# Performance work log

Hardware: AMD Instinct MI355X
Metric: run time of the kernel (lower is better)

Reference implementation:

```python
import jax, jax.numpy as jnp
import numpy as np

N = 100000   # nodes per node type
E = 1000000  # edges per edge type
C = 128      # channels
H = 4        # num_heads
D = C // H   # head_dim


def setup_inputs() -> dict:
    key = jax.random.key(0)
    ks = jax.random.split(key, 16)
    return {
        "x_A": jax.random.normal(ks[0], (N, C), jnp.float32),
        "x_B": jax.random.normal(ks[1], (N, C), jnp.float32),
        "Wq": jax.random.normal(ks[2], (C, C), jnp.float32) * 0.05,
        "bq": jax.random.normal(ks[3], (C,), jnp.float32) * 0.05,
        "Wk": jax.random.normal(ks[4], (C, C), jnp.float32) * 0.05,
        "bk": jax.random.normal(ks[5], (C,), jnp.float32) * 0.05,
        "Wv": jax.random.normal(ks[6], (C, C), jnp.float32) * 0.05,
        "bv": jax.random.normal(ks[7], (C,), jnp.float32) * 0.05,
        "gamma": jnp.ones((C,), jnp.float32),
        "beta": jnp.zeros((C,), jnp.float32),
        "bias_AB": jax.random.normal(ks[8], (1,), jnp.float32),
        "bias_BA": jax.random.normal(ks[9], (1,), jnp.float32),
        "sb_AB": jax.random.normal(ks[10], (E,), jnp.float32),
        "sb_BA": jax.random.normal(ks[11], (E,), jnp.float32),
        "edge_index_AB": jax.random.randint(ks[12], (2, E), 0, N, jnp.int32),
        "edge_index_BA": jax.random.randint(ks[13], (2, E), 0, N, jnp.int32),
    }


def _edge_attention(x_src, x_dst, src, dst, sb, etype_bias, Wq, bq, Wk, bk, Wv, bv):
    """Per-edge-type attention: gather -> score -> dst-segment softmax -> scatter-add."""
    n_dst = x_dst.shape[0]
    Q = (x_dst @ Wq.T + bq).reshape(n_dst, H, D)
    K = (x_src @ Wk.T + bk).reshape(-1, H, D)
    V = (x_src @ Wv.T + bv).reshape(-1, H, D)
    # [E, H] per-edge scores
    scores = jnp.einsum('ehd,ehd->eh', Q[dst], K[src]) / np.float32(np.sqrt(D))
    scores = scores + sb[:, None] + etype_bias  # spatial bias + edge-type bias
    # segment softmax over edges grouped by dst node (numerically stable)
    m = jax.ops.segment_max(scores, dst, num_segments=n_dst)
    ex = jnp.exp(scores - m[dst])
    denom = jax.ops.segment_sum(ex, dst, num_segments=n_dst)
    w = ex / denom[dst]  # [E, H]
    msg = (V[src] * w[:, :, None]).reshape(-1, C)  # [E, C]
    return jax.ops.segment_sum(msg, dst, num_segments=n_dst)  # index_add_


def _layernorm(x, gamma, beta, eps=1e-5):
    mu = x.mean(-1, keepdims=True)
    var = ((x - mu) ** 2).mean(-1, keepdims=True)
    return (x - mu) / jnp.sqrt(var + eps) * gamma + beta


def _forward(x_A, x_B, Wq, bq, Wk, bk, Wv, bv, gamma, beta,
             bias_AB, bias_BA, sb_AB, sb_BA, edge_index_AB, edge_index_BA):
    src_ab, dst_ab = edge_index_AB[0], edge_index_AB[1]  # A -> B
    src_ba, dst_ba = edge_index_BA[0], edge_index_BA[1]  # B -> A
    lin = (Wq, bq, Wk, bk, Wv, bv)
    out_B = _edge_attention(x_A, x_B, src_ab, dst_ab, sb_AB, bias_AB, *lin)
    out_A = _edge_attention(x_B, x_A, src_ba, dst_ba, sb_BA, bias_BA, *lin)
    # total degree = in_deg + out_deg per node type
    ones_e = jnp.ones((E,), jnp.float32)
    deg_A = (jax.ops.segment_sum(ones_e, src_ab, num_segments=N)
             + jax.ops.segment_sum(ones_e, dst_ba, num_segments=N))
    deg_B = (jax.ops.segment_sum(ones_e, dst_ab, num_segments=N)
             + jax.ops.segment_sum(ones_e, src_ba, num_segments=N))
    out_A = out_A + deg_A[:, None]
    out_B = out_B + deg_B[:, None]
    out_A = _layernorm(out_A + x_A, gamma, beta)
    out_B = _layernorm(out_B + x_B, gamma, beta)
    return out_A, out_B


def reference(x_A, x_B, Wq, bq, Wk, bk, Wv, bv, gamma, beta,
              bias_AB, bias_BA, sb_AB, sb_BA, edge_index_AB, edge_index_BA):
    return _forward(x_A, x_B, Wq, bq, Wk, bk, Wv, bv, gamma, beta,
                    bias_AB, bias_BA, sb_AB, sb_BA, edge_index_AB, edge_index_BA)
```

## Files before the change

### kernel.cpp

```cpp
#include <hip/hip_runtime.h>

#define CH 128
#define QSCALE (0.17677669529663687f * 1.4426950408889634f)
#define LOG2E 1.4426950408889634f
#define SCAN_BLK 1024
#define KVSTRIDE 384
#define QROWS 32

typedef _Float16 f16;
typedef _Float16 f16x2 __attribute__((ext_vector_type(2)));
typedef _Float16 f16x8 __attribute__((ext_vector_type(8)));
typedef __attribute__((ext_vector_type(4))) float f32x4;

__device__ __forceinline__ unsigned pk2(float a, float b) {
    auto h = __builtin_amdgcn_cvt_pkrtz(a, b);
    return __builtin_bit_cast(unsigned, h);
}
__device__ __forceinline__ f16x2 u2h(unsigned u) { return __builtin_bit_cast(f16x2, u); }

template <int CTRL>
__device__ __forceinline__ float dpp_add(float x) {
    const int t = __builtin_amdgcn_update_dpp(0, __builtin_bit_cast(int, x), CTRL, 0xF, 0xF, false);
    return x + __builtin_bit_cast(float, t);
}
__device__ __forceinline__ float head_sum(float x) {
    x = dpp_add<0xB1>(x);
    x = dpp_add<0x4E>(x);
    x = dpp_add<0x124>(x);
    x = dpp_add<0x128>(x);
    return x;
}

__global__ __launch_bounds__(256) void wcvt(const float* __restrict__ Wq, const float* __restrict__ Wk,
                                            const float* __restrict__ Wv, unsigned short* __restrict__ out)
{
    const int i = blockIdx.x * 256 + threadIdx.x;
    if (i >= 3 * CH * CH) return;
    const float* W = (i < CH * CH) ? Wq : (i < 2 * CH * CH) ? Wk : Wv;
    const float s = (i < CH * CH) ? QSCALE : 1.f;
    f16 h = (f16)(W[i & (CH * CH - 1)] * s);
    out[i] = __builtin_bit_cast(unsigned short, h);
}

__global__ __launch_bounds__(256) void qkv_mfma(
    const float* __restrict__ xA, const float* __restrict__ xB,
    const unsigned short* __restrict__ Wb,
    const float* __restrict__ bq, const float* __restrict__ bk, const float* __restrict__ bv,
    unsigned short* __restrict__ Qb,
    unsigned char* __restrict__ KVb,
    int n)
{
    __shared__ __align__(16) char lds[8192];
    const int type = blockIdx.y;
    const float* x = type ? xB : xA;
    const int bRow = blockIdx.x * QROWS;
    const int tid = threadIdx.x;

    #pragma unroll
    for (int j = 0; j < 4; ++j) {
        const int flat16 = j * 256 + tid;
        const int row = flat16 >> 5;
        const int c16 = flat16 & 31;
        float4 v = make_float4(0.f, 0.f, 0.f, 0.f);
        if (bRow + row < n) v = *(const float4*)(x + (size_t)(bRow + row) * CH + c16 * 4);
        const int off = (row * 256 + c16 * 8) ^ ((row & 7) << 4);
        *(uint2*)(lds + off) = make_uint2(pk2(v.x, v.y), pk2(v.z, v.w));
    }
    __syncthreads();

    const int w = tid >> 6, l = tid & 63, lr = l & 15, lg = l >> 4;
    const int colbase = w * 32;

    f32x4 acc[3][2][2];
    #pragma unroll
    for (int p = 0; p < 3; ++p)
        #pragma unroll
        for (int ct = 0; ct < 2; ++ct)
            #pragma unroll
            for (int rt = 0; rt < 2; ++rt)
                acc[p][ct][rt] = (f32x4){0.f, 0.f, 0.f, 0.f};

    #pragma unroll
    for (int kt = 0; kt < 4; ++kt) {
        f16x8 bx[2];
        #pragma unroll
        for (int rt = 0; rt < 2; ++rt) {
            const int row = rt * 16 + lr;
            const int off = (row * 256 + kt * 64 + lg * 16) ^ ((row & 7) << 4);
            bx[rt] = *(const f16x8*)(lds + off);
        }
        #pragma unroll
        for (int p = 0; p < 3; ++p) {
            #pragma unroll
            for (int ct = 0; ct < 2; ++ct) {
                const int ocol = colbase + ct * 16 + lr;
                const f16x8 a = *(const f16x8*)(Wb + ((size_t)p << 14) + (size_t)ocol * CH + kt * 32 + lg * 8);
                #pragma unroll
                for (int rt = 0; rt < 2; ++rt)
                    acc[p][ct][rt] = __builtin_amdgcn_mfma_f32_16x16x32_f16(a, bx[rt], acc[p][ct][rt], 0, 0, 0);
            }
        }
    }

    unsigned short* Qo = Qb + (size_t)type * n * CH;
    unsigned char* KVo = KVb + (size_t)type * n * KVSTRIDE;

    #pragma unroll
    for (int p = 0; p < 3; ++p) {
        __syncthreads();
        const float* bias = (p == 0) ? bq : (p == 1) ? bk : bv;
        #pragma unroll
        for (int ct = 0; ct < 2; ++ct) {
            const int c0 = colbase + ct * 16 + lg * 4;
            float4 bb = *(const float4*)(bias + c0);
            if (p == 0) { bb.x *= QSCALE; bb.y *= QSCALE; bb.z *= QSCALE; bb.w *= QSCALE; }
            #pragma unroll
            for (int rt = 0; rt < 2; ++rt) {
                const int nl = rt * 16 + lr;
                const int swz = (nl & 7) << 4;
                const f32x4 a4 = acc[p][ct][rt];
                if (p == 1) {
                    const int cbk = w * 32 + ct * 16 + lg * 4;
                    int kw = __builtin_amdgcn_cvt_pk_fp8_f32(a4[0] + bb.x, a4[1] + bb.y, 0, false);
                    kw     = __builtin_amdgcn_cvt_pk_fp8_f32(a4[2] + bb.z, a4[3] + bb.w, kw, true);
                    *(unsigned*)(lds + nl * 128 + (cbk ^ swz)) = (unsigned)kw;
                } else {
                    const int cbq = w * 64 + ct * 32 + lg * 8;
                    *(uint2*)(lds + nl * 256 + (cbq ^ swz)) =
                        make_uint2(pk2(a4[0] + bb.x, a4[1] + bb.y), pk2(a4[2] + bb.z, a4[3] + bb.w));
                }
            }
        }
        __syncthreads();
        if (p == 1) {
            const int row = tid >> 3, c = tid & 7;
            const uint4 val = *(const uint4*)(lds + row * 128 + ((c ^ (row & 7)) << 4));
            const int node = bRow + row;
            if (node < n) *(uint4*)(KVo + (size_t)node * KVSTRIDE + c * 16) = val;
        } else {
            #pragma unroll
            for (int j = 0; j < 2; ++j) {
                const int flat = j * 256 + tid;
                const int row = flat >> 4, c16 = flat & 15;
                const uint4 val = *(const uint4*)(lds + row * 256 + ((c16 ^ (row & 7)) << 4));
                const int node = bRow + row;
                if (node < n) {
                    if (p == 0) *(uint4*)(Qo + (size_t)node * CH + c16 * 8) = val;
                    else        *(uint4*)(KVo + (size_t)node * KVSTRIDE + 128 + c16 * 16) = val;
                }
            }
        }
    }
}

__global__ __launch_bounds__(256) void deg_hist(const int* __restrict__ eiAB, const int* __restrict__ eiBA,
                                                int* __restrict__ degAB, int* __restrict__ degBA,
                                                int nE, int ebl)
{
    const int dir = blockIdx.x >= ebl;
    const int e = ((blockIdx.x - dir * ebl) * 256 + threadIdx.x) * 4;
    if (e >= nE) return;
    const int* ei = dir ? eiBA : eiAB;
    int* deg = dir ? degBA : degAB;
    if (e + 3 < nE) {
        const int4 d4 = *(const int4*)(ei + nE + e);
        atomicAdd(&deg[d4.x], 1); atomicAdd(&deg[d4.y], 1);
        atomicAdd(&deg[d4.z], 1); atomicAdd(&deg[d4.w], 1);
    } else {
        for (int j = e; j < nE; ++j) atomicAdd(&deg[ei[nE + j]], 1);
    }
}

__global__ __launch_bounds__(256) void scan_local(const int* __restrict__ degAB, const int* __restrict__ degBA,
                                                  int* __restrict__ offsAB, int* __restrict__ offsBA,
                                                  int* __restrict__ bsums, int n, int nb)
{
    __shared__ int s[256];
    const int dir = blockIdx.x >= nb;
    const int blk = blockIdx.x - dir * nb;
    const int* deg = dir ? degBA : degAB;
    int* offs = dir ? offsBA : offsAB;
    int* bs = bsums + dir * 256;

    const int t = threadIdx.x;
    const int base = blk * SCAN_BLK + t * 4;
    int v0 = 0, v1 = 0, v2 = 0, v3 = 0;
    if (base + 3 < n) {
        int4 q = *(const int4*)(deg + base);
        v0 = q.x; v1 = q.y; v2 = q.z; v3 = q.w;
    } else {
        if (base + 0 < n) v0 = deg[base + 0];
        if (base + 1 < n) v1 = deg[base + 1];
        if (base + 2 < n) v2 = deg[base + 2];
    }
    const int tsum = v0 + v1 + v2 + v3;
    s[t] = tsum;
    __syncthreads();
    for (int off = 1; off < 256; off <<= 1) {
        int add = (t >= off) ? s[t - off] : 0;
        __syncthreads();
        s[t] += add;
        __syncthreads();
    }
    const int excl = s[t] - tsum;
    if (base + 0 < n) offs[base + 0] = excl;
    if (base + 1 < n) offs[base + 1] = excl + v0;
    if (base + 2 < n) offs[base + 2] = excl + v0 + v1;
    if (base + 3 < n) offs[base + 3] = excl + v0 + v1 + v2;
    if (t == 255) bs[blk] = s[255];
}

__global__ __launch_bounds__(256) void add_bsums(int* __restrict__ offsAB, int* __restrict__ offsBA,
                                                 int* __restrict__ curAB, int* __restrict__ curBA,
                                                 const int* __restrict__ bsums, int n, int nbl, int nb)
{
    __shared__ int s[256];
    const int dir = blockIdx.x >= nbl;
    const int blk = blockIdx.x - dir * nbl;
    const int t = threadIdx.x;
    int v = (t < nb) ? bsums[dir * 256 + t] : 0;
    s[t] = v;
    __syncthreads();
    for (int off = 1; off < 256; off <<= 1) {
        int add = (t >= off) ? s[t - off] : 0;
        __syncthreads();
        s[t] += add;
        __syncthreads();
    }
    const int i = blk * 256 + t;
    if (i >= n) return;
    const int bi = i >> 10;
    const int excl = (bi == 0) ? 0 : s[bi - 1];
    int* offs = dir ? offsBA : offsAB;
    int* cur  = dir ? curBA  : curAB;
    const int vv = offs[i] + excl;
    offs[i] = vv;
    cur[i] = vv;
}

__global__ __launch_bounds__(256) void csr_fill(const int* __restrict__ eiAB, const int* __restrict__ eiBA,
                                                const float* __restrict__ sbAB, const float* __restrict__ sbBA,
                                                const float* __restrict__ biasAB, const float* __restrict__ biasBA,
                                                int* __restrict__ curAB, int* __restrict__ curBA,
                                                int2* __restrict__ edAB, int2* __restrict__ edBA,
                                                int nE, int ebl)
{
    const int dir = blockIdx.x >= ebl;
    const int e = ((blockIdx.x - dir * ebl) * 256 + threadIdx.x) * 4;
    if (e >= nE) return;
    const int* ei = dir ? eiBA : eiAB;
    const float* sb = dir ? sbBA : sbAB;
    const float bia = dir ? biasBA[0] : biasAB[0];
    int* cur = dir ? curBA : curAB;
    int2* ed = dir ? edBA : edAB;
    if (e + 3 < nE) {
        const int4 s4 = *(const int4*)(ei + e);
        const int4 d4 = *(const int4*)(ei + nE + e);
        const float4 b4 = *(const float4*)(sb + e);
        int p0 = atomicAdd(&cur[d4.x], 1); ed[p0] = make_int2(s4.x * KVSTRIDE, __float_as_int((b4.x + bia) * LOG2E));
        int p1 = atomicAdd(&cur[d4.y], 1); ed[p1] = make_int2(s4.y * KVSTRIDE, __float_as_int((b4.y + bia) * LOG2E));
        int p2 = atomicAdd(&cur[d4.z], 1); ed[p2] = make_int2(s4.z * KVSTRIDE, __float_as_int((b4.z + bia) * LOG2E));
        int p3 = atomicAdd(&cur[d4.w], 1); ed[p3] = make_int2(s4.w * KVSTRIDE, __float_as_int((b4.w + bia) * LOG2E));
    } else {
        for (int j = e; j < nE; ++j) {
            const int pos = atomicAdd(&cur[ei[nE + j]], 1);
            ed[pos] = make_int2(ei[j] * KVSTRIDE, __float_as_int((sb[j] + bia) * LOG2E));
        }
    }
}

__global__ __launch_bounds__(256) void attn_node(
    const unsigned short* __restrict__ Qb,
    const unsigned char* __restrict__ KVb,
    const float* __restrict__ xA, const float* __restrict__ xB,
    const int* __restrict__ offsAB, const int* __restrict__ offsBA,
    const int* __restrict__ degAB, const int* __restrict__ degBA,
    const int2* __restrict__ edAB, const int2* __restrict__ edBA,
    const float* __restrict__ gamma, const float* __restrict__ beta,
    float* __restrict__ out, int n, int abl)
{
    const int dir = blockIdx.x >= abl;
    const int node = (blockIdx.x - dir * abl) * 4 + (threadIdx.x >> 6);
    if (node >= n) return;
    const int l = threadIdx.x & 63;
    const int l2 = l * 2;

    const unsigned short* Q = Qb + (size_t)dir * n * CH;
    const unsigned char* KV = KVb + (size_t)(1 - dir) * n * KVSTRIDE;
    const float* x = dir ? xB : xA;
    const int* offs = dir ? offsAB : offsBA;
    const int* deg  = dir ? degAB  : degBA;
    const int2* ed  = dir ? edAB   : edBA;
    float* o = out + (size_t)dir * n * CH;

    const f16x2 qp = u2h(*(const unsigned*)(Q + (size_t)node * CH + l2));
    const float qf0 = (float)qp[0], qf1 = (float)qp[1];

    const int beg = __builtin_amdgcn_readfirstlane(offs[node]);
    const int d   = __builtin_amdgcn_readfirstlane(deg[node]);

    float m = -3.0e38f, den = 0.f;
    f16x2 a01 = (f16x2){(f16)0.f, (f16)0.f};

    auto loadE = [&](int i, float& sbf, unsigned& kc, unsigned& vc) {
        if (i < d) {
            const int2 e = ed[beg + i];
            sbf = __int_as_float(e.y);
            const unsigned b = (unsigned)e.x;
            kc = *(const unsigned short*)(KV + b + l2);
            vc = *(const unsigned*)(KV + b + 128 + l2 * 2);
        } else {
            sbf = __int_as_float((int)0xFF800000u);
            kc = 0; vc = 0;
        }
    };

    auto procPair = [&](float sf0, unsigned k0, unsigned v0,
                        float sf1, unsigned k1, unsigned v1) {
        const auto kf0 = __builtin_amdgcn_cvt_pk_f32_fp8((int)k0, false);
        const auto kf1 = __builtin_amdgcn_cvt_pk_f32_fp8((int)k1, false);
        float sa = head_sum(fmaf(qf0, kf0[0], qf1 * kf0[1])) + sf0;
        float sb = head_sum(fmaf(qf0, kf1[0], qf1 * kf1[1])) + sf1;
        const float pm = fmaxf(sa, sb);
        if (!__all(pm <= m + 8.f)) {
            const float mn = fmaxf(m, pm);
            const float sc = exp2f(m - mn);
            den *= sc;
            a01 *= u2h(pk2(sc, sc));
            m = mn;
        }
        const float ea = exp2f(sa - m);
        const float eb = exp2f(sb - m);
        den += ea + eb;
        a01 += u2h(pk2(ea, ea)) * u2h(v0);
        a01 += u2h(pk2(eb, eb)) * u2h(v1);
    };

    float sA0, sA1, sA2, sA3, sB0, sB1, sB2, sB3;
    unsigned kA0, kA1, kA2, kA3, kB0, kB1, kB2, kB3;
    unsigned vA0, vA1, vA2, vA3, vB0, vB1, vB2, vB3;
    loadE(0, sA0, kA0, vA0); loadE(1, sA1, kA1, vA1);
    loadE(2, sA2, kA2, vA2); loadE(3, sA3, kA3, vA3);
    loadE(4, sB0, kB0, vB0); loadE(5, sB1, kB1, vB1);
    loadE(6, sB2, kB2, vB2); loadE(7, sB3, kB3, vB3);

    for (int i = 0; i < d; i += 8) {
        procPair(sA0, kA0, vA0, sA1, kA1, vA1);
        procPair(sA2, kA2, vA2, sA3, kA3, vA3);
        loadE(i + 8,  sA0, kA0, vA0); loadE(i + 9,  sA1, kA1, vA1);
        loadE(i + 10, sA2, kA2, vA2); loadE(i + 11, sA3, kA3, vA3);
        if (i + 4 >= d) break;
        procPair(sB0, kB0, vB0, sB1, kB1, vB1);
        procPair(sB2, kB2, vB2, sB3, kB3, vB3);
        loadE(i + 12, sB0, kB0, vB0); loadE(i + 13, sB1, kB1, vB1);
        loadE(i + 14, sB2, kB2, vB2); loadE(i + 15, sB3, kB3, vB3);
    }

    const float inv = (den > 0.f) ? 1.f / den : 0.f;
    const float2 xv = *(const float2*)(x + (size_t)node * CH + l2);
    const float w0 = (float)a01[0] * inv + xv.x;
    const float w1 = (float)a01[1] * inv + xv.y;

    float sum = w0 + w1;
    #pragma unroll
    for (int off = 32; off; off >>= 1) sum += __shfl_xor(sum, off);
    const float mean = sum * (1.f / 128.f);
    const float c0 = w0 - mean, c1 = w1 - mean;
    float vs = c0 * c0 + c1 * c1;
    #pragma unroll
    for (int off = 32; off; off >>= 1) vs += __shfl_xor(vs, off);
    const float rstd = rsqrtf(vs * (1.f / 128.f) + 1e-5f);

    const float2 g = *(const float2*)(gamma + l2);
    const float2 bt = *(const float2*)(beta + l2);
    float2 ov;
    ov.x = c0 * rstd * g.x + bt.x;
    ov.y = c1 * rstd * g.y + bt.y;
    *(float2*)(o + (size_t)node * CH + l2) = ov;
}

extern "C" void kernel_launch(void* const* d_in, const int* in_sizes, int n_in,
                              void* d_out, int out_size, void* d_ws, size_t ws_size,
                              hipStream_t stream)
{
    const float* xA     = (const float*)d_in[0];
    const float* xB     = (const float*)d_in[1];
    const float* Wq     = (const float*)d_in[2];
    const float* bq     = (const float*)d_in[3];
    const float* Wk     = (const float*)d_in[4];
    const float* bk     = (const float*)d_in[5];
    const float* Wv     = (const float*)d_in[6];
    const float* bv     = (const float*)d_in[7];
    const float* gamma  = (const float*)d_in[8];
    const float* beta   = (const float*)d_in[9];
    const float* biasAB = (const float*)d_in[10];
    const float* biasBA = (const float*)d_in[11];
    const float* sbAB   = (const float*)d_in[12];
    const float* sbBA   = (const float*)d_in[13];
    const int*   eiAB   = (const int*)d_in[14];
    const int*   eiBA   = (const int*)d_in[15];

    const int n  = in_sizes[0] / CH;
    const int nE = in_sizes[12];
    const size_t NC = (size_t)n * CH;

    char* p = (char*)d_ws;
    auto carve = [&](size_t bytes) { char* r = p; p += (bytes + 15) & ~(size_t)15; return r; };
    unsigned short* Qb = (unsigned short*)carve(2 * NC * 2);
    unsigned char*  KVb = (unsigned char*)carve((size_t)2 * n * KVSTRIDE);
    unsigned short* Wb  = (unsigned short*)carve(3 * CH * CH * 2);
    int2* edAB  = (int2*)carve((size_t)nE * 8);
    int2* edBA  = (int2*)carve((size_t)nE * 8);
    int* offsAB = (int*)carve((size_t)n * 4);
    int* offsBA = (int*)carve((size_t)n * 4);
    int* degAB  = (int*)carve((size_t)2 * n * 4);
    int* degBA  = degAB + n;
    int* curAB  = (int*)carve((size_t)n * 4);
    int* curBA  = (int*)carve((size_t)n * 4);
    int* bsums  = (int*)carve(2 * 256 * 4);

    float* out = (float*)d_out;

    (void)hipMemsetAsync(degAB, 0, (size_t)2 * n * sizeof(int), stream);

    wcvt<<<(3 * CH * CH + 255) / 256, 256, 0, stream>>>(Wq, Wk, Wv, Wb);

    const int ebl4 = (nE + 1023) / 1024;
    deg_hist<<<2 * ebl4, 256, 0, stream>>>(eiAB, eiBA, degAB, degBA, nE, ebl4);

    dim3 qkv_grid((n + QROWS - 1) / QROWS, 2);
    qkv_mfma<<<qkv_grid, 256, 0, stream>>>(xA, xB, Wb, bq, bk, bv, Qb, KVb, n);

    const int nb = (n + SCAN_BLK - 1) / SCAN_BLK;
    scan_local<<<2 * nb, 256, 0, stream>>>(degAB, degBA, offsAB, offsBA, bsums, n, nb);
    const int nbl = (n + 255) / 256;
    add_bsums<<<2 * nbl, 256, 0, stream>>>(offsAB, offsBA, curAB, curBA, bsums, n, nbl, nb);

    csr_fill<<<2 * ebl4, 256, 0, stream>>>(eiAB, eiBA, sbAB, sbBA, biasAB, biasBA,
                                           curAB, curBA, edAB, edBA, nE, ebl4);

    const int abl = (n + 3) / 4;
    attn_node<<<2 * abl, 256, 0, stream>>>(Qb, KVb, xA, xB, offsAB, offsBA, degAB, degBA,
                                           edAB, edBA, gamma, beta, out, n, abl);
}
```

Measured before the change: 508.3 us.

## Merge weight conversion with degree histogram and QKV GEMM with CSR fill

Folds the weight-conversion kernel into the degree-histogram launch, and runs the QKV MFMA projection and the CSR fill as disjoint block ranges of one launch. The goal is fewer kernel launches and letting the compute-bound GEMM overlap the atomic-bound scatter, which previously ran serially. The QKV grid is flattened, with the node type taken from the low bit of blockIdx. In exchange, the fused kernels carry the GEMM's shared-memory footprint on the scatter blocks, and blocks with different resource use now compete for the same CUs.

```diff
diff --git a/kernel.cpp b/kernel.cpp
--- a/kernel.cpp
+++ b/kernel.cpp
@@ -6,6 +6,7 @@
 #define SCAN_BLK 1024
 #define KVSTRIDE 384
 #define QROWS 32
+#define WCVT_BLOCKS 192
 
 typedef _Float16 f16;
 typedef _Float16 f16x2 __attribute__((ext_vector_type(2)));
@@ -31,29 +32,148 @@
     return x;
 }
 
-__global__ __launch_bounds__(256) void wcvt(const float* __restrict__ Wq, const float* __restrict__ Wk,
-                                            const float* __restrict__ Wv, unsigned short* __restrict__ out)
-{
-    const int i = blockIdx.x * 256 + threadIdx.x;
-    if (i >= 3 * CH * CH) return;
-    const float* W = (i < CH * CH) ? Wq : (i < 2 * CH * CH) ? Wk : Wv;
-    const float s = (i < CH * CH) ? QSCALE : 1.f;
-    f16 h = (f16)(W[i & (CH * CH - 1)] * s);
-    out[i] = __builtin_bit_cast(unsigned short, h);
-}
-
-__global__ __launch_bounds__(256) void qkv_mfma(
+__global__ __launch_bounds__(256) void wcvt_hist(
+    const float* __restrict__ Wq, const float* __restrict__ Wk, const float* __restrict__ Wv,
+    unsigned short* __restrict__ Wb,
+    const int* __restrict__ eiAB, const int* __restrict__ eiBA,
+    int* __restrict__ degAB, int* __restrict__ degBA,
+    int nE, int ebl)
+{
+    if ((int)blockIdx.x < WCVT_BLOCKS) {
+        const int i = blockIdx.x * 256 + threadIdx.x;
+        const float* W = (i < CH * CH) ? Wq : (i < 2 * CH * CH) ? Wk : Wv;
+        const float s = (i < CH * CH) ? QSCALE : 1.f;
+        f16 h = (f16)(W[i & (CH * CH - 1)] * s);
+        Wb[i] = __builtin_bit_cast(unsigned short, h);
+        return;
+    }
+    const int b = blockIdx.x - WCVT_BLOCKS;
+    const int dir = b >= ebl;
+    const int e = ((b - dir * ebl) * 256 + threadIdx.x) * 4;
+    if (e >= nE) return;
+    const int* ei = dir ? eiBA : eiAB;
+    int* deg = dir ? degBA : degAB;
+    if (e + 3 < nE) {
+        const int4 d4 = *(const int4*)(ei + nE + e);
+        atomicAdd(&deg[d4.x], 1); atomicAdd(&deg[d4.y], 1);
+        atomicAdd(&deg[d4.z], 1); atomicAdd(&deg[d4.w], 1);
+    } else {
+        for (int j = e; j < nE; ++j) atomicAdd(&deg[ei[nE + j]], 1);
+    }
+}
+
+__global__ __launch_bounds__(256) void scan_local(const int* __restrict__ degAB, const int* __restrict__ degBA,
+                                                  int* __restrict__ offsAB, int* __restrict__ offsBA,
+                                                  int* __restrict__ bsums, int n, int nb)
+{
+    __shared__ int s[256];
+    const int dir = blockIdx.x >= nb;
+    const int blk = blockIdx.x - dir * nb;
+    const int* deg = dir ? degBA : degAB;
+    int* offs = dir ? offsBA : offsAB;
+    int* bs = bsums + dir * 256;
+
+    const int t = threadIdx.x;
+    const int base = blk * SCAN_BLK + t * 4;
+    int v0 = 0, v1 = 0, v2 = 0, v3 = 0;
+    if (base + 3 < n) {
+        int4 q = *(const int4*)(deg + base);
+        v0 = q.x; v1 = q.y; v2 = q.z; v3 = q.w;
+    } else {
+        if (base + 0 < n) v0 = deg[base + 0];
+        if (base + 1 < n) v1 = deg[base + 1];
+        if (base + 2 < n) v2 = deg[base + 2];
+    }
+    const int tsum = v0 + v1 + v2 + v3;
+    s[t] = tsum;
+    __syncthreads();
+    for (int off = 1; off < 256; off <<= 1) {
+        int add = (t >= off) ? s[t - off] : 0;
+        __syncthreads();
+        s[t] += add;
+        __syncthreads();
+    }
+    const int excl = s[t] - tsum;
+    if (base + 0 < n) offs[base + 0] = excl;
+    if (base + 1 < n) offs[base + 1] = excl + v0;
+    if (base + 2 < n) offs[base + 2] = excl + v0 + v1;
+    if (base + 3 < n) offs[base + 3] = excl + v0 + v1 + v2;
+    if (t == 255) bs[blk] = s[255];
+}
+
+__global__ __launch_bounds__(256) void add_bsums(int* __restrict__ offsAB, int* __restrict__ offsBA,
+                                                 int* __restrict__ curAB, int* __restrict__ curBA,
+                                                 const int* __restrict__ bsums, int n, int nbl, int nb)
+{
+    __shared__ int s[256];
+    const int dir = blockIdx.x >= nbl;
+    const int blk = blockIdx.x - dir * nbl;
+    const int t = threadIdx.x;
+    int v = (t < nb) ? bsums[dir * 256 + t] : 0;
+    s[t] = v;
+    __syncthreads();
+    for (int off = 1; off < 256; off <<= 1) {
+        int add = (t >= off) ? s[t - off] : 0;
+        __syncthreads();
+        s[t] += add;
+        __syncthreads();
+    }
+    const int i = blk * 256 + t;
+    if (i >= n) return;
+    const int bi = i >> 10;
+    const int excl = (bi == 0) ? 0 : s[bi - 1];
+    int* offs = dir ? offsBA : offsAB;
+    int* cur  = dir ? curBA  : curAB;
+    const int vv = offs[i] + excl;
+    offs[i] = vv;
+    cur[i] = vv;
+}
+
+__global__ __launch_bounds__(256) void qkv_csr(
     const float* __restrict__ xA, const float* __restrict__ xB,
     const unsigned short* __restrict__ Wb,
     const float* __restrict__ bq, const float* __restrict__ bk, const float* __restrict__ bv,
     unsigned short* __restrict__ Qb,
     unsigned char* __restrict__ KVb,
-    int n)
+    const int* __restrict__ eiAB, const int* __restrict__ eiBA,
+    const float* __restrict__ sbAB, const float* __restrict__ sbBA,
+    const float* __restrict__ biasAB, const float* __restrict__ biasBA,
+    int* __restrict__ curAB, int* __restrict__ curBA,
+    int2* __restrict__ edAB, int2* __restrict__ edBA,
+    int n, int nE, int qblocks, int ebl)
 {
     __shared__ __align__(16) char lds[8192];
-    const int type = blockIdx.y;
+
+    if ((int)blockIdx.x >= qblocks) {
+        const int b = blockIdx.x - qblocks;
+        const int dir = b >= ebl;
+        const int e = ((b - dir * ebl) * 256 + threadIdx.x) * 4;
+        if (e >= nE) return;
+        const int* ei = dir ? eiBA : eiAB;
+        const float* sb = dir ? sbBA : sbAB;
+        const float bia = dir ? biasBA[0] : biasAB[0];
+        int* cur = dir ? curBA : curAB;
+        int2* ed = dir ? edBA : edAB;
+        if (e + 3 < nE) {
+            const int4 s4 = *(const int4*)(ei + e);
+            const int4 d4 = *(const int4*)(ei + nE + e);
+            const float4 b4 = *(const float4*)(sb + e);
+            int p0 = atomicAdd(&cur[d4.x], 1); ed[p0] = make_int2(s4.x * KVSTRIDE, __float_as_int((b4.x + bia) * LOG2E));
+            int p1 = atomicAdd(&cur[d4.y], 1); ed[p1] = make_int2(s4.y * KVSTRIDE, __float_as_int((b4.y + bia) * LOG2E));
+            int p2 = atomicAdd(&cur[d4.z], 1); ed[p2] = make_int2(s4.z * KVSTRIDE, __float_as_int((b4.z + bia) * LOG2E));
+            int p3 = atomicAdd(&cur[d4.w], 1); ed[p3] = make_int2(s4.w * KVSTRIDE, __float_as_int((b4.w + bia) * LOG2E));
+        } else {
+            for (int j = e; j < nE; ++j) {
+                const int pos = atomicAdd(&cur[ei[nE + j]], 1);
+                ed[pos] = make_int2(ei[j] * KVSTRIDE, __float_as_int((sb[j] + bia) * LOG2E));
+            }
+        }
+        return;
+    }
+
+    const int type = blockIdx.x & 1;
     const float* x = type ? xB : xA;
-    const int bRow = blockIdx.x * QROWS;
+    const int bRow = ((int)blockIdx.x >> 1) * QROWS;
     const int tid = threadIdx.x;
 
     #pragma unroll
@@ -153,122 +273,6 @@
     }
 }
 
-__global__ __launch_bounds__(256) void deg_hist(const int* __restrict__ eiAB, const int* __restrict__ eiBA,
-                                                int* __restrict__ degAB, int* __restrict__ degBA,
-                                                int nE, int ebl)
-{
-    const int dir = blockIdx.x >= ebl;
-    const int e = ((blockIdx.x - dir * ebl) * 256 + threadIdx.x) * 4;
-    if (e >= nE) return;
-    const int* ei = dir ? eiBA : eiAB;
-    int* deg = dir ? degBA : degAB;
-    if (e + 3 < nE) {
-        const int4 d4 = *(const int4*)(ei + nE + e);
-        atomicAdd(&deg[d4.x], 1); atomicAdd(&deg[d4.y], 1);
-        atomicAdd(&deg[d4.z], 1); atomicAdd(&deg[d4.w], 1);
-    } else {
-        for (int j = e; j < nE; ++j) atomicAdd(&deg[ei[nE + j]], 1);
-    }
-}
-
-__global__ __launch_bounds__(256) void scan_local(const int* __restrict__ degAB, const int* __restrict__ degBA,
-                                                  int* __restrict__ offsAB, int* __restrict__ offsBA,
-                                                  int* __restrict__ bsums, int n, int nb)
-{
-    __shared__ int s[256];
-    const int dir = blockIdx.x >= nb;
-    const int blk = blockIdx.x - dir * nb;
-    const int* deg = dir ? degBA : degAB;
-    int* offs = dir ? offsBA : offsAB;
-    int* bs = bsums + dir * 256;
-
-    const int t = threadIdx.x;
-    const int base = blk * SCAN_BLK + t * 4;
-    int v0 = 0, v1 = 0, v2 = 0, v3 = 0;
-    if (base + 3 < n) {
-        int4 q = *(const int4*)(deg + base);
-        v0 = q.x; v1 = q.y; v2 = q.z; v3 = q.w;
-    } else {
-        if (base + 0 < n) v0 = deg[base + 0];
-        if (base + 1 < n) v1 = deg[base + 1];
-        if (base + 2 < n) v2 = deg[base + 2];
-    }
-    const int tsum = v0 + v1 + v2 + v3;
-    s[t] = tsum;
-    __syncthreads();
-    for (int off = 1; off < 256; off <<= 1) {
-        int add = (t >= off) ? s[t - off] : 0;
-        __syncthreads();
-        s[t] += add;
-        __syncthreads();
-    }
-    const int excl = s[t] - tsum;
-    if (base + 0 < n) offs[base + 0] = excl;
-    if (base + 1 < n) offs[base + 1] = excl + v0;
-    if (base + 2 < n) offs[base + 2] = excl + v0 + v1;
-    if (base + 3 < n) offs[base + 3] = excl + v0 + v1 + v2;
-    if (t == 255) bs[blk] = s[255];
-}
-
-__global__ __launch_bounds__(256) void add_bsums(int* __restrict__ offsAB, int* __restrict__ offsBA,
-                                                 int* __restrict__ curAB, int* __restrict__ curBA,
-                                                 const int* __restrict__ bsums, int n, int nbl, int nb)
-{
-    __shared__ int s[256];
-    const int dir = blockIdx.x >= nbl;
-    const int blk = blockIdx.x - dir * nbl;
-    const int t = threadIdx.x;
-    int v = (t < nb) ? bsums[dir * 256 + t] : 0;
-    s[t] = v;
-    __syncthreads();
-    for (int off = 1; off < 256; off <<= 1) {
-        int add = (t >= off) ? s[t - off] : 0;
-        __syncthreads();
-        s[t] += add;
-        __syncthreads();
-    }
-    const int i = blk * 256 + t;
-    if (i >= n) return;
-    const int bi = i >> 10;
-    const int excl = (bi == 0) ? 0 : s[bi - 1];
-    int* offs = dir ? offsBA : offsAB;
-    int* cur  = dir ? curBA  : curAB;
-    const int vv = offs[i] + excl;
-    offs[i] = vv;
-    cur[i] = vv;
-}
-
-__global__ __launch_bounds__(256) void csr_fill(const int* __restrict__ eiAB, const int* __restrict__ eiBA,
-                                                const float* __restrict__ sbAB, const float* __restrict__ sbBA,
-                                                const float* __restrict__ biasAB, const float* __restrict__ biasBA,
-                                                int* __restrict__ curAB, int* __restrict__ curBA,
-                                                int2* __restrict__ edAB, int2* __restrict__ edBA,
-                                                int nE, int ebl)
-{
-    const int dir = blockIdx.x >= ebl;
-    const int e = ((blockIdx.x - dir * ebl) * 256 + threadIdx.x) * 4;
-    if (e >= nE) return;
-    const int* ei = dir ? eiBA : eiAB;
-    const float* sb = dir ? sbBA : sbAB;
-    const float bia = dir ? biasBA[0] : biasAB[0];
-    int* cur = dir ? curBA : curAB;
-    int2* ed = dir ? edBA : edAB;
-    if (e + 3 < nE) {
-        const int4 s4 = *(const int4*)(ei + e);
-        const int4 d4 = *(const int4*)(ei + nE + e);
-        const float4 b4 = *(const float4*)(sb + e);
-        int p0 = atomicAdd(&cur[d4.x], 1); ed[p0] = make_int2(s4.x * KVSTRIDE, __float_as_int((b4.x + bia) * LOG2E));
-        int p1 = atomicAdd(&cur[d4.y], 1); ed[p1] = make_int2(s4.y * KVSTRIDE, __float_as_int((b4.y + bia) * LOG2E));
-        int p2 = atomicAdd(&cur[d4.z], 1); ed[p2] = make_int2(s4.z * KVSTRIDE, __float_as_int((b4.z + bia) * LOG2E));
-        int p3 = atomicAdd(&cur[d4.w], 1); ed[p3] = make_int2(s4.w * KVSTRIDE, __float_as_int((b4.w + bia) * LOG2E));
-    } else {
-        for (int j = e; j < nE; ++j) {
-            const int pos = atomicAdd(&cur[ei[nE + j]], 1);
-            ed[pos] = make_int2(ei[j] * KVSTRIDE, __float_as_int((sb[j] + bia) * LOG2E));
-        }
-    }
-}
-
 __global__ __launch_bounds__(256) void attn_node(
     const unsigned short* __restrict__ Qb,
     const unsigned char* __restrict__ KVb,
@@ -423,21 +427,20 @@
 
     (void)hipMemsetAsync(degAB, 0, (size_t)2 * n * sizeof(int), stream);
 
-    wcvt<<<(3 * CH * CH + 255) / 256, 256, 0, stream>>>(Wq, Wk, Wv, Wb);
-
     const int ebl4 = (nE + 1023) / 1024;
-    deg_hist<<<2 * ebl4, 256, 0, stream>>>(eiAB, eiBA, degAB, degBA, nE, ebl4);
-
-    dim3 qkv_grid((n + QROWS - 1) / QROWS, 2);
-    qkv_mfma<<<qkv_grid, 256, 0, stream>>>(xA, xB, Wb, bq, bk, bv, Qb, KVb, n);
+    wcvt_hist<<<WCVT_BLOCKS + 2 * ebl4, 256, 0, stream>>>(Wq, Wk, Wv, Wb,
+                                                          eiAB, eiBA, degAB, degBA, nE, ebl4);
 
     const int nb = (n + SCAN_BLK - 1) / SCAN_BLK;
     scan_local<<<2 * nb, 256, 0, stream>>>(degAB, degBA, offsAB, offsBA, bsums, n, nb);
     const int nbl = (n + 255) / 256;
     add_bsums<<<2 * nbl, 256, 0, stream>>>(offsAB, offsBA, curAB, curBA, bsums, n, nbl, nb);
 
-    csr_fill<<<2 * ebl4, 256, 0, stream>>>(eiAB, eiBA, sbAB, sbBA, biasAB, biasBA,
-                                           curAB, curBA, edAB, edBA, nE, ebl4);
+    const int qblocks = 2 * ((n + QROWS - 1) / QROWS);
+    qkv_csr<<<qblocks + 2 * ebl4, 256, 0, stream>>>(xA, xB, Wb, bq, bk, bv, Qb, KVb,
+                                                    eiAB, eiBA, sbAB, sbBA, biasAB, biasBA,
+                                                    curAB, curBA, edAB, edBA,
+                                                    n, nE, qblocks, ebl4);
 
     const int abl = (n + 3) / 4;
     attn_node<<<2 * abl, 256, 0, stream>>>(Qb, KVb, xA, xB, offsAB, offsBA, degAB, degBA,
```

New measurement: 458.1 us. 9.9% less time.
